# Performance work log

Measured on AMD Instinct MI355X. Metric: run time of the kernel, lower is better.

Reference implementation:

```python
import jax, jax.numpy as jnp
import numpy as np

B, L, D, DFF, DLLM, E, TOPK = 16, 512, 768, 3072, 4096, 8, 2
EPS_GATE = 1e-9
LN_EPS = 1e-5


def _layernorm(x, gamma, beta):
    mu = jnp.mean(x, axis=-1, keepdims=True)
    var = jnp.var(x, axis=-1, keepdims=True)
    return (x - mu) * jax.lax.rsqrt(var + LN_EPS) * gamma + beta


def _mlp_block(x, w1, b1, w2, b2, gamma, beta):
    # MLPBlock: Linear -> GELU -> Linear -> LayerNorm(residual). Dropout is identity in eval.
    h = jax.nn.gelu(x @ w1 + b1)
    o = h @ w2 + b2
    return _layernorm(o + x, gamma, beta)


def setup_inputs() -> dict:
    key = jax.random.key(0)
    ks = jax.random.split(key, 24)
    sd = lambda fan_in: 1.0 / np.sqrt(fan_in)
    inp = {
        'cycle_curve_data': jax.random.normal(ks[0], (B, L, D), jnp.float32),
        'cycle_numbers': jax.random.uniform(ks[1], (B, 1), jnp.float32) * 1000.0,
        'DKP_embeddings': jax.random.normal(ks[2], (B, DLLM), jnp.float32),
        # Gate (PatternRouter_two): fuses LLM embedding + cycle number -> expert logits
        'gate_We': jax.random.normal(ks[3], (DLLM, DFF), jnp.float32) * sd(DLLM),
        'gate_Wc': jax.random.normal(ks[4], (1, DFF), jnp.float32),
        'gate_b': jnp.zeros((DFF,), jnp.float32),
        'gate_Wo': jax.random.normal(ks[5], (DFF, E), jnp.float32) * sd(DFF),
        'gate_bo': jnp.zeros((E,), jnp.float32),
        # Stacked expert params [E, ...]
        'e_w1': jax.random.normal(ks[6], (E, D, DFF), jnp.float32) * sd(D),
        'e_b1': jnp.zeros((E, DFF), jnp.float32),
        'e_w2': jax.random.normal(ks[7], (E, DFF, D), jnp.float32) * sd(DFF),
        'e_b2': jnp.zeros((E, D), jnp.float32),
        'e_gamma': jnp.ones((E, D), jnp.float32),
        'e_beta': jnp.zeros((E, D), jnp.float32),
        # General expert
        'g_w1': jax.random.normal(ks[8], (D, DFF), jnp.float32) * sd(D),
        'g_b1': jnp.zeros((DFF,), jnp.float32),
        'g_w2': jax.random.normal(ks[9], (DFF, D), jnp.float32) * sd(DFF),
        'g_b2': jnp.zeros((D,), jnp.float32),
        'g_gamma': jnp.ones((D,), jnp.float32),
        'g_beta': jnp.zeros((D,), jnp.float32),
    }
    return inp


def reference(cycle_curve_data, cycle_numbers, DKP_embeddings,
              gate_We, gate_Wc, gate_b, gate_Wo, gate_bo,
              e_w1, e_b1, e_w2, e_b2, e_gamma, e_beta,
              g_w1, g_b1, g_w2, g_b2, g_gamma, g_beta):
    # --- Router: clean logits (eval mode: no noise) ---
    h = jax.nn.relu(DKP_embeddings @ gate_We + cycle_numbers @ gate_Wc + gate_b)
    logits = h @ gate_Wo + gate_bo                         # [B, E]
    _, idx = jax.lax.top_k(logits, TOPK)                   # [B, TOPK]
    probs = jax.nn.softmax(logits, axis=1)
    mask = jnp.zeros_like(probs).at[jnp.arange(B)[:, None], idx].set(1.0)
    gated = probs * mask
    gated = gated / (jnp.sum(gated, axis=1, keepdims=True) + EPS_GATE)  # [B, E]

    # --- Experts: dense compute, zero gates zero out non-routed experts ---
    x = cycle_curve_data
    combined = jnp.zeros_like(x)
    for e in range(E):  # small fixed expert count
        out_e = _mlp_block(x, e_w1[e], e_b1[e], e_w2[e], e_b2[e], e_gamma[e], e_beta[e])
        combined = combined + gated[:, e, None, None] * out_e

    general = _mlp_block(x, g_w1, g_b1, g_w2, g_b2, g_gamma, g_beta)
    final_out = general + combined.astype(jnp.bfloat16)  # matches .to(torch.bfloat16) cast before add
    return final_out
```

## Files before the change

kernel.cpp:

```cpp
#include <hip/hip_runtime.h>
#include <cstdint>

#define B_    16
#define L_    512
#define D_    768
#define DFF_  3072
#define DLLM_ 4096
#define E_    8

typedef unsigned short ushort_t;
typedef __attribute__((ext_vector_type(4))) float accfrag_t;
typedef __attribute__((ext_vector_type(8))) short bfrag_t;

typedef __attribute__((address_space(3))) uint32_t lds_u32;
typedef __attribute__((address_space(1))) uint32_t glb_u32;

__device__ inline void gload16(const void* g, void* l) {
  __builtin_amdgcn_global_load_lds((const glb_u32*)(uintptr_t)g,
                                   (lds_u32*)(uint32_t)(uintptr_t)l, 16, 0, 0);
}

__device__ inline ushort_t f2bf(float f) {
  uint32_t u = __float_as_uint(f);
  return (ushort_t)((u + 0x7FFFu + ((u >> 16) & 1u)) >> 16);
}
__device__ inline float bf2f(ushort_t v) { return __uint_as_float(((uint32_t)v) << 16); }

#define MFMA16(a, b, c) __builtin_amdgcn_mfma_f32_16x16x32_bf16(a, b, c, 0, 0, 0)

template <int KT>
__device__ __forceinline__ void gemm_body(const char* gA, const char* gB,
                                          char* sm, accfrag_t acc[4][4]) {
  const int tid = threadIdx.x;
  const int lane = tid & 63;
  const int w = tid >> 6, wm = w >> 1, wn = w & 1;
  const int LDB = KT * 128;

  const int R0 = tid >> 3;
  const char* srcA = gA + (size_t)R0 * LDB + ((((tid & 7) ^ (R0 & 7)) << 4));
  const char* srcB = gB + (size_t)R0 * LDB + ((((tid & 7) ^ (R0 & 7)) << 4));
  const int dl = tid * 16;

  const int l15 = lane & 15, l7 = lane & 7, lhi = lane >> 4;
  const int a0 = (wm * 64 + l15) * 128 + ((lhi ^ l7) << 4);
  const int a1 = (wm * 64 + l15) * 128 + (((4 + lhi) ^ l7) << 4);
  const int b0 = 16384 + (wn * 64 + l15) * 128 + ((lhi ^ l7) << 4);
  const int b1 = 16384 + (wn * 64 + l15) * 128 + (((4 + lhi) ^ l7) << 4);

#pragma unroll 1
  for (int t = 0; t < KT; ++t) {
    const size_t ko = (size_t)t * 128;
#pragma unroll
    for (int j = 0; j < 4; ++j)
      gload16(srcA + (size_t)j * 32 * LDB + ko, sm + j * 4096 + dl);
#pragma unroll
    for (int j = 0; j < 4; ++j)
      gload16(srcB + (size_t)j * 32 * LDB + ko, sm + 16384 + j * 4096 + dl);
    __syncthreads();
    bfrag_t af0[4], af1[4], bf0[4], bf1[4];
#pragma unroll
    for (int nf = 0; nf < 4; ++nf) {
      bf0[nf] = *(const bfrag_t*)(sm + b0 + nf * 2048);
      bf1[nf] = *(const bfrag_t*)(sm + b1 + nf * 2048);
    }
#pragma unroll
    for (int mf = 0; mf < 4; ++mf) {
      af0[mf] = *(const bfrag_t*)(sm + a0 + mf * 2048);
      af1[mf] = *(const bfrag_t*)(sm + a1 + mf * 2048);
    }
    __builtin_amdgcn_s_setprio(1);
#pragma unroll
    for (int mf = 0; mf < 4; ++mf)
#pragma unroll
      for (int nf = 0; nf < 4; ++nf) {
        acc[mf][nf] = MFMA16(af0[mf], bf0[nf], acc[mf][nf]);
        acc[mf][nf] = MFMA16(af1[mf], bf1[nf], acc[mf][nf]);
      }
    __builtin_amdgcn_s_setprio(0);
    __syncthreads();
  }
}

__device__ inline void job_tile(int f, int tilesPerJob, int jp_count,
                                int& jobIdx, int& t) {
  if ((jp_count & 7) == 0) {
    const int xcd = f & 7, slot = f >> 3;
    jobIdx = xcd + 8 * (slot / tilesPerJob);
    t = slot % tilesPerJob;
  } else {
    jobIdx = f / tilesPerJob;
    t = f % tilesPerJob;
  }
}

__global__ __launch_bounds__(256, 3)
void gemm1_k(const ushort_t* __restrict__ xb, const ushort_t* __restrict__ w1t,
             const float* __restrict__ e_b1, const float* __restrict__ g_b1,
             const int* __restrict__ tidx, ushort_t* __restrict__ h_out,
             int job0, int jp_count) {
  __shared__ char sm[32768];
  int jp, t;
  job_tile(blockIdx.x, 96, jp_count, jp, t);
  const int mt = t / 24, nt = t % 24;
  const int job = job0 + jp;
  const int b = job / 3, s = job - b * 3;
  const int e = (s < 2) ? tidx[b * 2 + s] : E_;
  const char* gA = (const char*)(xb + ((size_t)b * L_ + mt * 128) * D_);
  const char* gB = (const char*)(w1t + ((size_t)e * DFF_ + nt * 128) * D_);
  accfrag_t acc[4][4] = {};
  gemm_body<12>(gA, gB, sm, acc);

  const float* b1 = (s < 2) ? (e_b1 + (size_t)e * DFF_) : g_b1;
  const int lane = threadIdx.x & 63, w = threadIdx.x >> 6;
  const int wm = w >> 1, wn = w & 1;
  const int row0 = mt * 128 + wm * 64 + ((lane >> 4) << 2);
  const int col0 = nt * 128 + wn * 64 + (lane & 15);
  float bias[4];
#pragma unroll
  for (int nf = 0; nf < 4; ++nf) bias[nf] = b1[col0 + nf * 16];
  ushort_t* hp = h_out + (size_t)jp * L_ * DFF_ + (size_t)row0 * DFF_ + col0;
#pragma unroll
  for (int mf = 0; mf < 4; ++mf)
#pragma unroll
    for (int r = 0; r < 4; ++r) {
      ushort_t* hr_ = hp + (size_t)(mf * 16 + r) * DFF_;
#pragma unroll
      for (int nf = 0; nf < 4; ++nf) {
        float v = acc[mf][nf][r] + bias[nf];
        float u = 0.7978845608028654f * (v + 0.044715f * v * v * v);
        float th = 1.0f - 2.0f / (1.0f + __expf(2.0f * u));
        hr_[nf * 16] = f2bf(0.5f * v * (1.0f + th));
      }
    }
}

__global__ __launch_bounds__(256, 3)
void gemm2_k(const ushort_t* __restrict__ h_in, const ushort_t* __restrict__ w2t,
             const float* __restrict__ e_b2, const float* __restrict__ g_b2,
             const float* __restrict__ x_f, const int* __restrict__ tidx,
             ushort_t* __restrict__ slot_o, float* __restrict__ outp,
             int job0, int jp_count) {
  __shared__ char sm[32768];
  int jp, t;
  job_tile(blockIdx.x, 24, jp_count, jp, t);
  const int mt = t / 6, nt = t % 6;
  const int job = job0 + jp;
  const int b = job / 3, s = job - b * 3;
  const int e = (s < 2) ? tidx[b * 2 + s] : E_;
  const char* gA = (const char*)(h_in + ((size_t)jp * L_ + mt * 128) * DFF_);
  const char* gB = (const char*)(w2t + ((size_t)e * D_ + nt * 128) * DFF_);
  accfrag_t acc[4][4] = {};
  gemm_body<48>(gA, gB, sm, acc);

  const float* b2 = (s < 2) ? (e_b2 + (size_t)e * D_) : g_b2;
  const int lane = threadIdx.x & 63, w = threadIdx.x >> 6;
  const int wm = w >> 1, wn = w & 1;
  const int row0 = mt * 128 + wm * 64 + ((lane >> 4) << 2);
  const int col0 = nt * 128 + wn * 64 + (lane & 15);
  float bias[4];
#pragma unroll
  for (int nf = 0; nf < 4; ++nf) bias[nf] = b2[col0 + nf * 16];
#pragma unroll
  for (int mf = 0; mf < 4; ++mf)
#pragma unroll
    for (int r = 0; r < 4; ++r) {
      const int row = row0 + mf * 16 + r;
      const float* xr = x_f + ((size_t)b * L_ + row) * D_ + col0;
#pragma unroll
      for (int nf = 0; nf < 4; ++nf) {
        float v = acc[mf][nf][r] + bias[nf] + xr[nf * 16];
        if (s < 2)
          slot_o[(((size_t)b * 2 + s) * L_ + row) * D_ + col0 + nf * 16] = f2bf(v);
        else
          outp[((size_t)b * L_ + row) * D_ + col0 + nf * 16] = v;
      }
    }
}

__global__ __launch_bounds__(256)
void transpose_cvt_k(const float* __restrict__ srcE, const float* __restrict__ srcG,
                     ushort_t* __restrict__ dst, int R, int C) {
  const int z = blockIdx.z;
  const float* src = (z < 8) ? (srcE + (size_t)z * R * C) : srcG;
  ushort_t* out = dst + (size_t)z * R * C;
  __shared__ float tile[64][65];
  const int c0 = blockIdx.x * 64, r0 = blockIdx.y * 64;
  const int t = threadIdx.x;
  const int rr = t >> 4, cc = (t & 15) * 4;
#pragma unroll
  for (int i = 0; i < 4; ++i) {
    const float4 v = *(const float4*)(src + (size_t)(r0 + rr + i * 16) * C + c0 + cc);
    tile[rr + i * 16][cc] = v.x; tile[rr + i * 16][cc + 1] = v.y;
    tile[rr + i * 16][cc + 2] = v.z; tile[rr + i * 16][cc + 3] = v.w;
  }
  __syncthreads();
  const int c = t >> 2, r8 = (t & 3) * 16;
#pragma unroll
  for (int j = 0; j < 2; ++j) {
    ushort_t u[8];
#pragma unroll
    for (int k = 0; k < 8; ++k) u[k] = f2bf(tile[r8 + j * 8 + k][c]);
    *(uint4*)(out + (size_t)(c0 + c) * R + r0 + r8 + j * 8) = *(const uint4*)u;
  }
}

__global__ void cvt_x_k(const float* __restrict__ in, ushort_t* __restrict__ out) {
  const int i = (blockIdx.x * 256 + threadIdx.x) * 4;
  const float4 v = *(const float4*)(in + i);
  uint2 u;
  u.x = (uint32_t)f2bf(v.x) | ((uint32_t)f2bf(v.y) << 16);
  u.y = (uint32_t)f2bf(v.z) | ((uint32_t)f2bf(v.w) << 16);
  *(uint2*)(out + i) = u;
}

__global__ __launch_bounds__(256)
void router_partial_k(const float* __restrict__ emb, const float* __restrict__ We,
                      float* __restrict__ rp) {
  const int nt = blockIdx.x, kb = blockIdx.y;
  const int tid = threadIdx.x;
  __shared__ float semb[B_][256];
  const int k0 = kb * 256;
#pragma unroll
  for (int r = 0; r < B_; ++r) semb[r][tid] = emb[(size_t)r * DLLM_ + k0 + tid];
  __syncthreads();
  const int f = nt * 256 + tid;
  float acc[B_] = {};
  for (int k = 0; k < 256; ++k) {
    const float wv = We[(size_t)(k0 + k) * DFF_ + f];
#pragma unroll
    for (int j = 0; j < B_; ++j) acc[j] += semb[j][k] * wv;
  }
#pragma unroll
  for (int j = 0; j < B_; ++j)
    rp[((size_t)kb * B_ + j) * DFF_ + f] = acc[j];
}

__global__ void router_reduce_k(const float* __restrict__ rp, const float* __restrict__ cyc,
                                const float* __restrict__ Wc, const float* __restrict__ gb,
                                float* __restrict__ hr) {
  const int g = blockIdx.x * 256 + threadIdx.x;
  const int b = g / DFF_, f = g - b * DFF_;
  float s = 0.0f;
#pragma unroll
  for (int kb = 0; kb < 16; ++kb)
    s += rp[((size_t)kb * B_ + b) * DFF_ + f];
  s += cyc[b] * Wc[f] + gb[f];
  hr[(size_t)b * DFF_ + f] = fmaxf(s, 0.0f);
}

__global__ void router_final_k(const float* __restrict__ hr, const float* __restrict__ Wo,
                               const float* __restrict__ bo, int* __restrict__ tidx,
                               float* __restrict__ gates) {
  const int b = blockIdx.x, tid = threadIdx.x;
  float acc[E_] = {};
  for (int f = tid; f < DFF_; f += 256) {
    const float hv = hr[(size_t)b * DFF_ + f];
#pragma unroll
    for (int o = 0; o < E_; ++o) acc[o] += hv * Wo[(size_t)f * E_ + o];
  }
  __shared__ float lred[E_][4];
#pragma unroll
  for (int o = 0; o < E_; ++o) {
    float v = acc[o];
#pragma unroll
    for (int off = 32; off > 0; off >>= 1) v += __shfl_down(v, off, 64);
    if ((tid & 63) == 0) lred[o][tid >> 6] = v;
  }
  __syncthreads();
  if (tid == 0) {
    float lg[E_];
    float mx = -1e30f;
    for (int o = 0; o < E_; ++o) {
      lg[o] = lred[o][0] + lred[o][1] + lred[o][2] + lred[o][3] + bo[o];
      mx = fmaxf(mx, lg[o]);
    }
    int i1 = 0;
    for (int o = 1; o < E_; ++o) if (lg[o] > lg[i1]) i1 = o;
    int i2 = (i1 == 0) ? 1 : 0;
    for (int o = 0; o < E_; ++o) if (o != i1 && lg[o] > lg[i2]) i2 = o;
    float p[E_], sum = 0.0f;
    for (int o = 0; o < E_; ++o) { p[o] = __expf(lg[o] - mx); sum += p[o]; }
    const float p1 = p[i1] / sum, p2 = p[i2] / sum;
    const float den = p1 + p2 + 1e-9f;
    tidx[b * 2] = i1; tidx[b * 2 + 1] = i2;
    gates[b * 2] = p1 / den; gates[b * 2 + 1] = p2 / den;
  }
}

__global__ __launch_bounds__(256)
void final_ln_k(float* __restrict__ outp, const ushort_t* __restrict__ so,
                const float* __restrict__ gates, const int* __restrict__ tidx,
                const float* __restrict__ e_gam, const float* __restrict__ e_bet,
                const float* __restrict__ g_gam, const float* __restrict__ g_bet) {
  const int row = blockIdx.x;
  const int b = row >> 9, l = row & 511;
  const int tid = threadIdx.x;
  __shared__ float red4[4];
  float* gr = outp + (size_t)row * D_;
  const ushort_t* s0 = so + (((size_t)b * 2 + 0) * L_ + l) * D_;
  const ushort_t* s1 = so + (((size_t)b * 2 + 1) * L_ + l) * D_;
  float a0[3], a1[3], a2[3];
#pragma unroll
  for (int j = 0; j < 3; ++j) {
    const int d = tid + j * 256;
    a0[j] = gr[d];
    a1[j] = bf2f(s0[d]);
    a2[j] = bf2f(s1[d]);
  }
  auto bsum = [&](float v) -> float {
#pragma unroll
    for (int o = 32; o > 0; o >>= 1) v += __shfl_down(v, o, 64);
    if ((tid & 63) == 0) red4[tid >> 6] = v;
    __syncthreads();
    const float r = red4[0] + red4[1] + red4[2] + red4[3];
    __syncthreads();
    return r;
  };
  const float sg = bsum(a0[0] + a0[1] + a0[2]);
  const float qg = bsum(a0[0] * a0[0] + a0[1] * a0[1] + a0[2] * a0[2]);
  const float s0s = bsum(a1[0] + a1[1] + a1[2]);
  const float q0s = bsum(a1[0] * a1[0] + a1[1] * a1[1] + a1[2] * a1[2]);
  const float s1s = bsum(a2[0] + a2[1] + a2[2]);
  const float q1s = bsum(a2[0] * a2[0] + a2[1] * a2[1] + a2[2] * a2[2]);
  const float inv = 1.0f / 768.0f;
  const float mug = sg * inv, rg = rsqrtf(qg * inv - mug * mug + 1e-5f);
  const float mu0 = s0s * inv, r0 = rsqrtf(q0s * inv - mu0 * mu0 + 1e-5f);
  const float mu1 = s1s * inv, r1 = rsqrtf(q1s * inv - mu1 * mu1 + 1e-5f);
  const int e0 = tidx[b * 2], e1 = tidx[b * 2 + 1];
  const float g0 = gates[b * 2], g1 = gates[b * 2 + 1];
#pragma unroll
  for (int j = 0; j < 3; ++j) {
    const int d = tid + j * 256;
    const float lng = (a0[j] - mug) * rg * g_gam[d] + g_bet[d];
    const float ln0 = (a1[j] - mu0) * r0 * e_gam[(size_t)e0 * D_ + d] + e_bet[(size_t)e0 * D_ + d];
    const float ln1 = (a2[j] - mu1) * r1 * e_gam[(size_t)e1 * D_ + d] + e_bet[(size_t)e1 * D_ + d];
    const float comb = g0 * ln0 + g1 * ln1;
    gr[d] = lng + bf2f(f2bf(comb));
  }
}

extern "C" void kernel_launch(void* const* d_in, const int* in_sizes, int n_in,
                              void* d_out, int out_size, void* d_ws, size_t ws_size,
                              hipStream_t stream) {
  const float* x_f  = (const float*)d_in[0];
  const float* cyc  = (const float*)d_in[1];
  const float* emb  = (const float*)d_in[2];
  const float* We   = (const float*)d_in[3];
  const float* Wc   = (const float*)d_in[4];
  const float* gb   = (const float*)d_in[5];
  const float* Wo   = (const float*)d_in[6];
  const float* bo   = (const float*)d_in[7];
  const float* e_w1 = (const float*)d_in[8];
  const float* e_b1 = (const float*)d_in[9];
  const float* e_w2 = (const float*)d_in[10];
  const float* e_b2 = (const float*)d_in[11];
  const float* e_gam = (const float*)d_in[12];
  const float* e_bet = (const float*)d_in[13];
  const float* g_w1 = (const float*)d_in[14];
  const float* g_b1 = (const float*)d_in[15];
  const float* g_w2 = (const float*)d_in[16];
  const float* g_b2 = (const float*)d_in[17];
  const float* g_gam = (const float*)d_in[18];
  const float* g_bet = (const float*)d_in[19];
  float* outp = (float*)d_out;
  char* ws = (char*)d_ws;

  size_t off = 0;
  auto alloc = [&](size_t bytes) { size_t o = off; off = (off + bytes + 255) & ~(size_t)255; return o; };
  const size_t o_idx  = alloc(32 * 4);
  const size_t o_gate = alloc(32 * 4);
  const size_t o_hr   = alloc((size_t)B_ * DFF_ * 4);
  const size_t o_rp   = alloc((size_t)16 * B_ * DFF_ * 4);
  const size_t o_xb   = alloc((size_t)B_ * L_ * D_ * 2);
  const size_t o_w1t  = alloc((size_t)9 * DFF_ * D_ * 2);
  const size_t o_w2t  = alloc((size_t)9 * D_ * DFF_ * 2);
  const size_t o_so   = alloc((size_t)B_ * 2 * L_ * D_ * 2);
  const size_t o_h    = off;

  int JP = 1;
  const int divs[10] = {48, 24, 16, 12, 8, 6, 4, 3, 2, 1};
  for (int k = 0; k < 10; ++k) {
    if (o_h + (size_t)divs[k] * L_ * DFF_ * 2 <= ws_size) { JP = divs[k]; break; }
  }

  ushort_t* xb    = (ushort_t*)(ws + o_xb);
  ushort_t* w1t   = (ushort_t*)(ws + o_w1t);
  ushort_t* w2t   = (ushort_t*)(ws + o_w2t);
  ushort_t* so    = (ushort_t*)(ws + o_so);
  ushort_t* h_ws  = (ushort_t*)(ws + o_h);
  int*      tidx  = (int*)(ws + o_idx);
  float*    gates = (float*)(ws + o_gate);
  float*    hr    = (float*)(ws + o_hr);
  float*    rp    = (float*)(ws + o_rp);

  cvt_x_k<<<dim3((B_ * L_ * D_) / 1024), dim3(256), 0, stream>>>(x_f, xb);
  transpose_cvt_k<<<dim3(DFF_ / 64, D_ / 64, 9), dim3(256), 0, stream>>>(e_w1, g_w1, w1t, D_, DFF_);
  transpose_cvt_k<<<dim3(D_ / 64, DFF_ / 64, 9), dim3(256), 0, stream>>>(e_w2, g_w2, w2t, DFF_, D_);
  router_partial_k<<<dim3(12, 16), dim3(256), 0, stream>>>(emb, We, rp);
  router_reduce_k<<<dim3(192), dim3(256), 0, stream>>>(rp, cyc, Wc, gb, hr);
  router_final_k<<<dim3(16), dim3(256), 0, stream>>>(hr, Wo, bo, tidx, gates);

  const int passes = 48 / JP;
  for (int p = 0; p < passes; ++p) {
    gemm1_k<<<dim3(96 * JP), dim3(256), 0, stream>>>(xb, w1t, e_b1, g_b1, tidx, h_ws, p * JP, JP);
    gemm2_k<<<dim3(24 * JP), dim3(256), 0, stream>>>(h_ws, w2t, e_b2, g_b2, x_f, tidx, so, outp, p * JP, JP);
  }
  final_ln_k<<<dim3(B_ * L_), dim3(256), 0, stream>>>(outp, so, gates, tidx,
                                                      e_gam, e_bet, g_gam, g_bet);
}
```

Baseline: 474.5 us.

## Switch expert GEMMs to 256x256 tiles with 8 waves and double-buffered LDS pipeline

Replaces the 128x128, 4-wave, single-buffered GEMM mainloop with 256x256 tiles computed by 8 waves (512 threads), using 128 KB of dynamic LDS split into two buffers. Loads for the next K-tile are issued in quarter-sized pieces between MFMA groups, gated by vmcnt waits and barriers, so global loads overlap compute. Larger tiles raise arithmetic intensity per byte loaded. In exchange occupancy drops to one block per CU, grid sizes shrink (gemm2 gets only 6 blocks per job), and wave-level tail effects may grow.

```diff
diff --git a/kernel.cpp b/kernel.cpp
--- a/kernel.cpp
+++ b/kernel.cpp
@@ -28,57 +28,87 @@
 
 #define MFMA16(a, b, c) __builtin_amdgcn_mfma_f32_16x16x32_bf16(a, b, c, 0, 0, 0)
 
+#define G_GATE(N)                                                           \
+  asm volatile("s_waitcnt vmcnt(" N ")" ::: "memory");                      \
+  __builtin_amdgcn_s_barrier();                                             \
+  asm volatile("" ::: "memory");
+
+#define G_STAGE_A(T, MQ)                                                    \
+  { char* d_ = sm + (((T)&1) << 16) + ((MQ) << 14) + (tid << 4);            \
+    const char* s_ = A_src + (size_t)((MQ) * 64) * LDB + (size_t)(T) * 128; \
+    gload16(s_, d_);                                                        \
+    gload16(s_ + (size_t)128 * LDB, d_ + 8192); }
+
+#define G_STAGE_B(T, NQ)                                                    \
+  { char* d_ = sm + (((T)&1) << 16) + 32768 + ((NQ) << 14) + (tid << 4);    \
+    const char* s_ = B_src + (size_t)((NQ) * 32) * LDB + (size_t)(T) * 128; \
+    gload16(s_, d_);                                                        \
+    gload16(s_ + (size_t)128 * LDB, d_ + 8192); }
+
+#define G_RDA(AR, SB, MQ)                                                   \
+  _Pragma("unroll") for (int m_ = 0; m_ < 4; ++m_) {                        \
+    AR[m_][0] = *(const bfrag_t*)((SB) + ((MQ) << 14) + aRow + m_ * 2048 + c0); \
+    AR[m_][1] = *(const bfrag_t*)((SB) + ((MQ) << 14) + aRow + m_ * 2048 + c1); }
+
+#define G_RDB(BR, SB, NQ)                                                   \
+  _Pragma("unroll") for (int n_ = 0; n_ < 2; ++n_) {                        \
+    BR[n_][0] = *(const bfrag_t*)((SB) + ((NQ) << 14) + bRow + n_ * 2048 + c0); \
+    BR[n_][1] = *(const bfrag_t*)((SB) + ((NQ) << 14) + bRow + n_ * 2048 + c1); }
+
+#define G_MF(AR, BR, MB, NB)                                                \
+  _Pragma("unroll") for (int m_ = 0; m_ < 4; ++m_)                          \
+    _Pragma("unroll") for (int n_ = 0; n_ < 2; ++n_) {                      \
+      acc[(MB)+m_][(NB)+n_] = MFMA16(AR[m_][0], BR[n_][0], acc[(MB)+m_][(NB)+n_]); \
+      acc[(MB)+m_][(NB)+n_] = MFMA16(AR[m_][1], BR[n_][1], acc[(MB)+m_][(NB)+n_]); }
+
+#define G_TILE(T, GATE, DOST)                                               \
+  { const char* sb_ = sm + (((T)&1) << 16);                                 \
+    G_GATE(GATE)                                                            \
+    G_RDA(a0f, sb_, 0) G_RDB(bf_, sb_, 0)                                   \
+    if (DOST) G_STAGE_A((T)+1, 0)                                           \
+    __builtin_amdgcn_s_setprio(1); G_MF(a0f, bf_, 0, 0)                     \
+    __builtin_amdgcn_s_setprio(0);                                          \
+    G_GATE(GATE)                                                            \
+    G_RDA(a1f, sb_, 1)                                                      \
+    if (DOST) G_STAGE_B((T)+1, 0)                                           \
+    __builtin_amdgcn_s_setprio(1); G_MF(a1f, bf_, 4, 0)                     \
+    __builtin_amdgcn_s_setprio(0);                                          \
+    G_GATE(GATE)                                                            \
+    G_RDB(bf_, sb_, 1)                                                      \
+    if (DOST) G_STAGE_A((T)+1, 1)                                           \
+    __builtin_amdgcn_s_setprio(1); G_MF(a1f, bf_, 4, 2)                     \
+    __builtin_amdgcn_s_setprio(0);                                          \
+    G_GATE(GATE)                                                            \
+    if (DOST) G_STAGE_B((T)+1, 1)                                           \
+    __builtin_amdgcn_s_setprio(1); G_MF(a0f, bf_, 0, 2)                     \
+    __builtin_amdgcn_s_setprio(0);                                          \
+  }
+
 template <int KT>
 __device__ __forceinline__ void gemm_body(const char* gA, const char* gB,
-                                          char* sm, accfrag_t acc[4][4]) {
+                                          char* sm, accfrag_t acc[8][4]) {
   const int tid = threadIdx.x;
   const int lane = tid & 63;
-  const int w = tid >> 6, wm = w >> 1, wn = w & 1;
+  const int w = tid >> 6, wm = w >> 2, wn = w & 3;
   const int LDB = KT * 128;
 
-  const int R0 = tid >> 3;
-  const char* srcA = gA + (size_t)R0 * LDB + ((((tid & 7) ^ (R0 & 7)) << 4));
-  const char* srcB = gB + (size_t)R0 * LDB + ((((tid & 7) ^ (R0 & 7)) << 4));
-  const int dl = tid * 16;
-
-  const int l15 = lane & 15, l7 = lane & 7, lhi = lane >> 4;
-  const int a0 = (wm * 64 + l15) * 128 + ((lhi ^ l7) << 4);
-  const int a1 = (wm * 64 + l15) * 128 + (((4 + lhi) ^ l7) << 4);
-  const int b0 = 16384 + (wn * 64 + l15) * 128 + ((lhi ^ l7) << 4);
-  const int b1 = 16384 + (wn * 64 + l15) * 128 + (((4 + lhi) ^ l7) << 4);
-
+  const int r3 = tid >> 3;
+  const int swz = (((tid & 7) ^ (r3 & 7)) << 4);
+  const char* A_src = gA + (size_t)r3 * LDB + swz;
+  const int g0row = ((r3 >> 5) << 6) + (r3 & 31);
+  const char* B_src = gB + (size_t)g0row * LDB + swz;
+
+  const int l15 = lane & 15, lhi = lane >> 4, l7 = lane & 7;
+  const int c0 = ((lhi ^ l7) << 4), c1 = (((4 + lhi) ^ l7) << 4);
+  const int aRow = (wm * 64 + l15) * 128;
+  const int bRow = 32768 + (wn * 32 + l15) * 128;
+
+  bfrag_t a0f[4][2], a1f[4][2], bf_[2][2];
+
+  G_STAGE_A(0, 0) G_STAGE_B(0, 0) G_STAGE_A(0, 1) G_STAGE_B(0, 1)
 #pragma unroll 1
-  for (int t = 0; t < KT; ++t) {
-    const size_t ko = (size_t)t * 128;
-#pragma unroll
-    for (int j = 0; j < 4; ++j)
-      gload16(srcA + (size_t)j * 32 * LDB + ko, sm + j * 4096 + dl);
-#pragma unroll
-    for (int j = 0; j < 4; ++j)
-      gload16(srcB + (size_t)j * 32 * LDB + ko, sm + 16384 + j * 4096 + dl);
-    __syncthreads();
-    bfrag_t af0[4], af1[4], bf0[4], bf1[4];
-#pragma unroll
-    for (int nf = 0; nf < 4; ++nf) {
-      bf0[nf] = *(const bfrag_t*)(sm + b0 + nf * 2048);
-      bf1[nf] = *(const bfrag_t*)(sm + b1 + nf * 2048);
-    }
-#pragma unroll
-    for (int mf = 0; mf < 4; ++mf) {
-      af0[mf] = *(const bfrag_t*)(sm + a0 + mf * 2048);
-      af1[mf] = *(const bfrag_t*)(sm + a1 + mf * 2048);
-    }
-    __builtin_amdgcn_s_setprio(1);
-#pragma unroll
-    for (int mf = 0; mf < 4; ++mf)
-#pragma unroll
-      for (int nf = 0; nf < 4; ++nf) {
-        acc[mf][nf] = MFMA16(af0[mf], bf0[nf], acc[mf][nf]);
-        acc[mf][nf] = MFMA16(af1[mf], bf1[nf], acc[mf][nf]);
-      }
-    __builtin_amdgcn_s_setprio(0);
-    __syncthreads();
-  }
+  for (int t = 0; t < KT - 1; ++t) G_TILE(t, "4", 1)
+  G_TILE(KT - 1, "0", 0)
 }
 
 __device__ inline void job_tile(int f, int tilesPerJob, int jp_count,
@@ -93,34 +123,34 @@
   }
 }
 
-__global__ __launch_bounds__(256, 3)
+__global__ __launch_bounds__(512, 1)
 void gemm1_k(const ushort_t* __restrict__ xb, const ushort_t* __restrict__ w1t,
              const float* __restrict__ e_b1, const float* __restrict__ g_b1,
              const int* __restrict__ tidx, ushort_t* __restrict__ h_out,
              int job0, int jp_count) {
-  __shared__ char sm[32768];
+  extern __shared__ char sm[];
   int jp, t;
-  job_tile(blockIdx.x, 96, jp_count, jp, t);
-  const int mt = t / 24, nt = t % 24;
+  job_tile(blockIdx.x, 24, jp_count, jp, t);
+  const int mt = t / 12, nt = t % 12;
   const int job = job0 + jp;
   const int b = job / 3, s = job - b * 3;
   const int e = (s < 2) ? tidx[b * 2 + s] : E_;
-  const char* gA = (const char*)(xb + ((size_t)b * L_ + mt * 128) * D_);
-  const char* gB = (const char*)(w1t + ((size_t)e * DFF_ + nt * 128) * D_);
-  accfrag_t acc[4][4] = {};
+  const char* gA = (const char*)(xb + ((size_t)b * L_ + mt * 256) * D_);
+  const char* gB = (const char*)(w1t + ((size_t)e * DFF_ + nt * 256) * D_);
+  accfrag_t acc[8][4] = {};
   gemm_body<12>(gA, gB, sm, acc);
 
   const float* b1 = (s < 2) ? (e_b1 + (size_t)e * DFF_) : g_b1;
   const int lane = threadIdx.x & 63, w = threadIdx.x >> 6;
-  const int wm = w >> 1, wn = w & 1;
-  const int row0 = mt * 128 + wm * 64 + ((lane >> 4) << 2);
-  const int col0 = nt * 128 + wn * 64 + (lane & 15);
+  const int wm = w >> 2, wn = w & 3;
+  const int row0 = mt * 256 + wm * 128 + ((lane >> 4) << 2);
+  const int col0 = nt * 256 + wn * 64 + (lane & 15);
   float bias[4];
 #pragma unroll
   for (int nf = 0; nf < 4; ++nf) bias[nf] = b1[col0 + nf * 16];
   ushort_t* hp = h_out + (size_t)jp * L_ * DFF_ + (size_t)row0 * DFF_ + col0;
 #pragma unroll
-  for (int mf = 0; mf < 4; ++mf)
+  for (int mf = 0; mf < 8; ++mf)
 #pragma unroll
     for (int r = 0; r < 4; ++r) {
       ushort_t* hr_ = hp + (size_t)(mf * 16 + r) * DFF_;
@@ -134,34 +164,34 @@
     }
 }
 
-__global__ __launch_bounds__(256, 3)
+__global__ __launch_bounds__(512, 1)
 void gemm2_k(const ushort_t* __restrict__ h_in, const ushort_t* __restrict__ w2t,
              const float* __restrict__ e_b2, const float* __restrict__ g_b2,
              const float* __restrict__ x_f, const int* __restrict__ tidx,
              ushort_t* __restrict__ slot_o, float* __restrict__ outp,
              int job0, int jp_count) {
-  __shared__ char sm[32768];
+  extern __shared__ char sm[];
   int jp, t;
-  job_tile(blockIdx.x, 24, jp_count, jp, t);
-  const int mt = t / 6, nt = t % 6;
+  job_tile(blockIdx.x, 6, jp_count, jp, t);
+  const int mt = t / 3, nt = t % 3;
   const int job = job0 + jp;
   const int b = job / 3, s = job - b * 3;
   const int e = (s < 2) ? tidx[b * 2 + s] : E_;
-  const char* gA = (const char*)(h_in + ((size_t)jp * L_ + mt * 128) * DFF_);
-  const char* gB = (const char*)(w2t + ((size_t)e * D_ + nt * 128) * DFF_);
-  accfrag_t acc[4][4] = {};
+  const char* gA = (const char*)(h_in + ((size_t)jp * L_ + mt * 256) * DFF_);
+  const char* gB = (const char*)(w2t + ((size_t)e * D_ + nt * 256) * DFF_);
+  accfrag_t acc[8][4] = {};
   gemm_body<48>(gA, gB, sm, acc);
 
   const float* b2 = (s < 2) ? (e_b2 + (size_t)e * D_) : g_b2;
   const int lane = threadIdx.x & 63, w = threadIdx.x >> 6;
-  const int wm = w >> 1, wn = w & 1;
-  const int row0 = mt * 128 + wm * 64 + ((lane >> 4) << 2);
-  const int col0 = nt * 128 + wn * 64 + (lane & 15);
+  const int wm = w >> 2, wn = w & 3;
+  const int row0 = mt * 256 + wm * 128 + ((lane >> 4) << 2);
+  const int col0 = nt * 256 + wn * 64 + (lane & 15);
   float bias[4];
 #pragma unroll
   for (int nf = 0; nf < 4; ++nf) bias[nf] = b2[col0 + nf * 16];
 #pragma unroll
-  for (int mf = 0; mf < 4; ++mf)
+  for (int mf = 0; mf < 8; ++mf)
 #pragma unroll
     for (int r = 0; r < 4; ++r) {
       const int row = row0 + mf * 16 + r;
@@ -393,6 +423,9 @@
   float*    hr    = (float*)(ws + o_hr);
   float*    rp    = (float*)(ws + o_rp);
 
+  hipFuncSetAttribute((const void*)gemm1_k, hipFuncAttributeMaxDynamicSharedMemorySize, 131072);
+  hipFuncSetAttribute((const void*)gemm2_k, hipFuncAttributeMaxDynamicSharedMemorySize, 131072);
+
   cvt_x_k<<<dim3((B_ * L_ * D_) / 1024), dim3(256), 0, stream>>>(x_f, xb);
   transpose_cvt_k<<<dim3(DFF_ / 64, D_ / 64, 9), dim3(256), 0, stream>>>(e_w1, g_w1, w1t, D_, DFF_);
   transpose_cvt_k<<<dim3(D_ / 64, DFF_ / 64, 9), dim3(256), 0, stream>>>(e_w2, g_w2, w2t, DFF_, D_);
@@ -402,8 +435,8 @@
 
   const int passes = 48 / JP;
   for (int p = 0; p < passes; ++p) {
-    gemm1_k<<<dim3(96 * JP), dim3(256), 0, stream>>>(xb, w1t, e_b1, g_b1, tidx, h_ws, p * JP, JP);
-    gemm2_k<<<dim3(24 * JP), dim3(256), 0, stream>>>(h_ws, w2t, e_b2, g_b2, x_f, tidx, so, outp, p * JP, JP);
+    gemm1_k<<<dim3(24 * JP), dim3(512), 131072, stream>>>(xb, w1t, e_b1, g_b1, tidx, h_ws, p * JP, JP);
+    gemm2_k<<<dim3(6 * JP), dim3(512), 131072, stream>>>(h_ws, w2t, e_b2, g_b2, x_f, tidx, so, outp, p * JP, JP);
   }
   final_ln_k<<<dim3(B_ * L_), dim3(256), 0, stream>>>(outp, so, gates, tidx,
                                                       e_gam, e_bet, g_gam, g_bet);
```

After: 539.7 us. 1.14x slower.
